# Optimization experiments

Measured on AMD Instinct MI355X. Metric: run time of the kernel, lower is better.

The kernel has to match this reference:

```python
import jax, jax.numpy as jnp
import numpy as np

DIM = 1024
N_HEADS = 16
HEAD_DIM = DIM // N_HEADS
B, N, M = 2, 2048, 2048


def setup_inputs() -> dict:
    key = jax.random.key(0)
    ks = jax.random.split(key, 10)
    s = 1.0 / np.sqrt(DIM)
    return {
        "x1": jax.random.normal(ks[0], (B, N, DIM), dtype=jnp.float32),
        "x2": jax.random.normal(ks[1], (B, M, DIM), dtype=jnp.float32),
        "Wq": jax.random.normal(ks[2], (DIM, DIM), dtype=jnp.float32) * s,
        "bq": jnp.zeros((DIM,), dtype=jnp.float32),
        "Wk": jax.random.normal(ks[3], (DIM, DIM), dtype=jnp.float32) * s,
        "bk": jnp.zeros((DIM,), dtype=jnp.float32),
        "Wv": jax.random.normal(ks[4], (DIM, DIM), dtype=jnp.float32) * s,
        "bv": jnp.zeros((DIM,), dtype=jnp.float32),
        "Wo": jax.random.normal(ks[5], (DIM, DIM), dtype=jnp.float32) * s,
        "bo": jnp.zeros((DIM,), dtype=jnp.float32),
    }


def reference(x1, x2, Wq, bq, Wk, bk, Wv, bv, Wo, bo):
    b, n, _ = x1.shape
    m = x2.shape[1]
    # projections (Linear: x @ W^T + b)
    q = x1 @ Wq.T + bq  # [b, n, dim]
    k = x2 @ Wk.T + bk  # [b, m, dim]
    v = x2 @ Wv.T + bv  # [b, m, dim]
    # split heads -> [b, h, seq, head_dim]
    q = q.reshape(b, n, N_HEADS, HEAD_DIM).transpose(0, 2, 1, 3)
    k = k.reshape(b, m, N_HEADS, HEAD_DIM).transpose(0, 2, 1, 3)
    v = v.reshape(b, m, N_HEADS, HEAD_DIM).transpose(0, 2, 1, 3)
    scale = 1.0 / jnp.sqrt(jnp.asarray(HEAD_DIM, dtype=q.dtype))
    scores = jnp.einsum('bhnd,bhmd->bhnm', q, k) * scale  # [b, h, n, m]
    attn = jax.nn.softmax(scores, axis=-1)
    o = jnp.einsum('bhnm,bhmd->bhnd', attn, v)  # [b, h, n, head_dim]
    o = o.transpose(0, 2, 1, 3).reshape(b, n, DIM)  # merge heads
    return o @ Wo.T + bo
```

## Files before the change

kernel.cpp:

```cpp
#include <hip/hip_runtime.h>
#include <stdint.h>

typedef unsigned short u16;
typedef __attribute__((ext_vector_type(4))) float f32x4;
typedef __attribute__((ext_vector_type(16))) float f32x16;
typedef __attribute__((ext_vector_type(8))) __bf16 bf16x8;
typedef __attribute__((ext_vector_type(8))) unsigned short u16x8;
typedef __attribute__((ext_vector_type(4))) unsigned short u16x4;

#define DIM_    1024
#define NHEADS_ 16
#define HD_     64
#define BB_     2
#define NN_     2048
#define MM_     2048

#define QSCALE 0.180336884f

__device__ inline u16 f32_to_bf16u(float f) {
  union { float f; uint32_t u; } x; x.f = f;
  uint32_t r = x.u + 0x7FFFu + ((x.u >> 16) & 1u);
  return (u16)(r >> 16);
}

__device__ inline void gload_lds16(const u16* g, u16* l) {
  u16* gnc = const_cast<u16*>(g);
  __builtin_amdgcn_global_load_lds(
      (__attribute__((address_space(1))) void*)gnc,
      (__attribute__((address_space(3))) void*)l, 16, 0, 0);
}

__device__ inline uint32_t cvt_pk_bf16(float lo, float hi) {
  uint32_t r;
  asm("v_cvt_pk_bf16_f32 %0, %1, %2" : "=v"(r) : "v"(lo), "v"(hi));
  return r;
}
__device__ inline void permlane32_swap(uint32_t& a, uint32_t& b) {
  asm("v_permlane32_swap_b32 %0, %1" : "+v"(a), "+v"(b));
}

__global__ void cast_all(const float* s0, u16* d0, const float* s1, u16* d1,
                         const float* s2, u16* d2, const float* s3, u16* d3,
                         const float* s4, u16* d4, const float* s5, u16* d5) {
  const float* s; u16* d; int n4;
  switch (blockIdx.y) {
    case 0: s = s0; d = d0; n4 = (BB_ * NN_ * DIM_) / 4; break;
    case 1: s = s1; d = d1; n4 = (BB_ * MM_ * DIM_) / 4; break;
    case 2: s = s2; d = d2; n4 = (DIM_ * DIM_) / 4; break;
    case 3: s = s3; d = d3; n4 = (DIM_ * DIM_) / 4; break;
    case 4: s = s4; d = d4; n4 = (DIM_ * DIM_) / 4; break;
    default: s = s5; d = d5; n4 = (DIM_ * DIM_) / 4; break;
  }
  int stride = gridDim.x * blockDim.x;
  for (int i = blockIdx.x * blockDim.x + threadIdx.x; i < n4; i += stride) {
    float4 f = reinterpret_cast<const float4*>(s)[i];
    u16x4 u;
    u.x = f32_to_bf16u(f.x);
    u.y = f32_to_bf16u(f.y);
    u.z = f32_to_bf16u(f.z);
    u.w = f32_to_bf16u(f.w);
    reinterpret_cast<u16x4*>(d)[i] = u;
  }
}

#define BM 128
#define BN 128
#define BK 64

template <bool BF16OUT>
__device__ __forceinline__
void gemm_body(const u16* __restrict__ A, const u16* __restrict__ Bm,
               const float* __restrict__ bias, void* __restrict__ Cout,
               int M, int N, int K, float scale,
               u16* As , u16* Bs ) {
  const int tid  = threadIdx.x;
  const int lane = tid & 63;
  const int wid  = tid >> 6;
  const int wr = wid >> 2, wc = wid & 3;
  const int fr = lane & 15, fq = lane >> 4;
  const int bm = blockIdx.x, bn = blockIdx.y;
  const int lrow = lane >> 3;
  const int scol = (((lane & 7) ^ lrow) * 8);

  f32x4 acc[4][2];
  #pragma unroll
  for (int m = 0; m < 4; ++m)
    #pragma unroll
    for (int n = 0; n < 2; ++n)
      acc[m][n] = f32x4{0.f, 0.f, 0.f, 0.f};

  const int NT = K / BK;

  auto stage = [&](int buf, int t) {
    int k0 = t * BK;
    #pragma unroll
    for (int c = 0; c < 2; ++c) {
      int ch  = wid * 2 + c;
      int row = ch * 8 + lrow;
      gload_lds16(A  + (size_t)(bm * BM + row) * K + k0 + scol, &As[buf * BM * BK + ch * 512]);
      gload_lds16(Bm + (size_t)(bn * BN + row) * K + k0 + scol, &Bs[buf * BN * BK + ch * 512]);
    }
  };

  stage(0, 0);
  __syncthreads();
  int cur = 0;
  for (int t = 0; t < NT; ++t) {
    if (t + 1 < NT) stage(cur ^ 1, t + 1);
    #pragma unroll
    for (int ks = 0; ks < 2; ++ks) {
      bf16x8 af[4], bfr[2];
      #pragma unroll
      for (int m = 0; m < 4; ++m)
        af[m] = *reinterpret_cast<const bf16x8*>(
            &As[cur * BM * BK + (wr * 64 + m * 16 + fr) * BK + (((ks * 4 + fq) ^ (fr & 7)) * 8)]);
      #pragma unroll
      for (int n = 0; n < 2; ++n)
        bfr[n] = *reinterpret_cast<const bf16x8*>(
            &Bs[cur * BN * BK + (wc * 32 + n * 16 + fr) * BK + (((ks * 4 + fq) ^ (fr & 7)) * 8)]);
      __builtin_amdgcn_s_setprio(1);
      #pragma unroll
      for (int m = 0; m < 4; ++m)
        #pragma unroll
        for (int n = 0; n < 2; ++n)
          acc[m][n] = __builtin_amdgcn_mfma_f32_16x16x32_bf16(af[m], bfr[n], acc[m][n], 0, 0, 0);
      __builtin_amdgcn_s_setprio(0);
    }
    __syncthreads();
    cur ^= 1;
  }

  #pragma unroll
  for (int n = 0; n < 2; ++n) {
    int col = bn * BN + wc * 32 + n * 16 + fr;
    float bv = bias[col];
    #pragma unroll
    for (int m = 0; m < 4; ++m) {
      #pragma unroll
      for (int i = 0; i < 4; ++i) {
        int row = bm * BM + wr * 64 + m * 16 + fq * 4 + i;
        float v = (acc[m][n][i] + bv) * scale;
        if (BF16OUT)
          ((u16*)Cout)[(size_t)row * N + col] = f32_to_bf16u(v);
        else
          ((float*)Cout)[(size_t)row * N + col] = v;
      }
    }
  }
}

__global__ __launch_bounds__(512)
void gemm_qkv(const u16* __restrict__ x1b, const u16* __restrict__ x2b,
              const u16* __restrict__ Wqb, const float* __restrict__ bq, u16* qb,
              const u16* __restrict__ Wkb, const float* __restrict__ bk, u16* kb,
              const u16* __restrict__ Wvb, const float* __restrict__ bv, u16* vb) {
  __shared__ __align__(16) u16 As[2 * BM * BK];
  __shared__ __align__(16) u16 Bs[2 * BN * BK];
  const u16* A; const u16* W; const float* bias; u16* C; float scale;
  switch (blockIdx.z) {
    case 0:  A = x1b; W = Wqb; bias = bq; C = qb; scale = QSCALE; break;
    case 1:  A = x2b; W = Wkb; bias = bk; C = kb; scale = 1.0f;   break;
    default: A = x2b; W = Wvb; bias = bv; C = vb; scale = 1.0f;   break;
  }
  gemm_body<true>(A, W, bias, C, BB_ * NN_, DIM_, DIM_, scale, As, Bs);
}

__global__ __launch_bounds__(512)
void gemm_o(const u16* __restrict__ A, const u16* __restrict__ W,
            const float* __restrict__ bias, float* __restrict__ C) {
  __shared__ __align__(16) u16 As[2 * BM * BK];
  __shared__ __align__(16) u16 Bs[2 * BN * BK];
  gemm_body<false>(A, W, bias, C, BB_ * NN_, DIM_, DIM_, 1.0f, As, Bs);
}

#define QB 128
#define KVB 64

__global__ __launch_bounds__(512)
void attn_fwd(const u16* __restrict__ qg, const u16* __restrict__ kg,
              const u16* __restrict__ vg, u16* __restrict__ og) {
  __shared__ __align__(16) u16 Ks[4][KVB * HD_];
  __shared__ __align__(16) u16 VTs[4][HD_ * KVB];
  const int tid = threadIdx.x, lane = tid & 63, wid = tid >> 6;
  const int hi = lane >> 5;
  const int l31 = lane & 31;
  const int wq = wid >> 1, wk = wid & 1;

  int lin = blockIdx.x + gridDim.x * (blockIdx.y + gridDim.y * blockIdx.z);
  int xcd = lin & 7, slot = lin >> 3;
  int r = slot & 15, gg2 = slot >> 4;
  int g = xcd + 8 * gg2;
  int h = g & 15, b = g >> 4;

  const size_t base_q  = (size_t)b * NN_ * DIM_ + (size_t)h * HD_;
  const size_t base_kv = (size_t)b * MM_ * DIM_ + (size_t)h * HD_;
  const int lrow = lane >> 3;
  const int scol = (((lane & 7) ^ lrow) * 8);

  bf16x8 qf[4];
  const int qrow = r * QB + wq * 32 + l31;
  #pragma unroll
  for (int step = 0; step < 4; ++step)
    qf[step] = *reinterpret_cast<const bf16x8*>(
        qg + base_q + (size_t)qrow * DIM_ + step * 16 + hi * 8);

  f32x16 oacc[2];
  #pragma unroll
  for (int dgrp = 0; dgrp < 2; ++dgrp)
    #pragma unroll
    for (int rg = 0; rg < 16; ++rg) oacc[dgrp][rg] = 0.f;
  float l_run = 0.f;

  const int NT = MM_ / KVB;

  auto stageK = [&](int buf, int t) {
    int kv0 = t * KVB;
    int row = wid * 8 + lrow;
    gload_lds16(kg + base_kv + (size_t)(kv0 + row) * DIM_ + scol, &Ks[buf][wid * 512]);
  };
  auto loadV = [&](int t, u16x8& vpre) {
    int kv0 = t * KVB;
    vpre = *reinterpret_cast<const u16x8*>(vg + base_kv + (size_t)(kv0 + lane) * DIM_ + wid * 8);
  };
  auto writeVT = [&](int buf, const u16x8& vpre) {
    #pragma unroll
    for (int j = 0; j < 8; ++j)
      VTs[buf][(wid * 8 + j) * KVB + (((lane >> 3) ^ j) * 8) + (lane & 7)] = vpre[j];
  };

  union PB { uint32_t w[4]; bf16x8 v; };

  auto compute = [&](int buf) {
    f32x16 s;
    #pragma unroll
    for (int rg = 0; rg < 16; ++rg) s[rg] = 0.f;
    __builtin_amdgcn_s_setprio(1);
    #pragma unroll
    for (int step = 0; step < 4; ++step) {
      bf16x8 kf = *reinterpret_cast<const bf16x8*>(
          (const char*)&Ks[buf][0] + (wk * 32 + l31) * 128 + (((step * 2 + hi) ^ (lane & 7)) * 16));
      s = __builtin_amdgcn_mfma_f32_32x32x16_bf16(kf, qf[step], s, 0, 0, 0);
    }
    __builtin_amdgcn_s_setprio(0);

    float p[16];
    #pragma unroll
    for (int rg = 0; rg < 16; ++rg) p[rg] = __builtin_amdgcn_exp2f(s[rg]);
    float lp = 0.f;
    #pragma unroll
    for (int rg = 0; rg < 16; ++rg) lp += p[rg];
    l_run += lp;

    PB pb[2];
    #pragma unroll
    for (int u = 0; u < 2; ++u) {
      uint32_t x0 = cvt_pk_bf16(p[u * 8 + 0], p[u * 8 + 1]);
      uint32_t y0 = cvt_pk_bf16(p[u * 8 + 4], p[u * 8 + 5]);
      permlane32_swap(x0, y0);
      uint32_t x1 = cvt_pk_bf16(p[u * 8 + 2], p[u * 8 + 3]);
      uint32_t y1 = cvt_pk_bf16(p[u * 8 + 6], p[u * 8 + 7]);
      permlane32_swap(x1, y1);
      pb[u].w[0] = x0; pb[u].w[1] = x1; pb[u].w[2] = y0; pb[u].w[3] = y1;
    }

    __builtin_amdgcn_s_setprio(1);
    #pragma unroll
    for (int dgrp = 0; dgrp < 2; ++dgrp)
      #pragma unroll
      for (int u = 0; u < 2; ++u) {
        bf16x8 vf = *reinterpret_cast<const bf16x8*>(
            (const char*)&VTs[buf][0] + (dgrp * 32 + l31) * 128 +
            (((wk * 4 + u * 2 + hi) ^ (lane & 7)) * 16));
        oacc[dgrp] = __builtin_amdgcn_mfma_f32_32x32x16_bf16(vf, pb[u].v, oacc[dgrp], 0, 0, 0);
      }
    __builtin_amdgcn_s_setprio(0);
  };

  {
    u16x8 v0, v1;
    loadV(0, v0);
    loadV(1, v1);
    stageK(0, 0);
    stageK(1, 1);
    writeVT(0, v0);
    writeVT(1, v1);
    __syncthreads();
  }

  for (int it = 0; it < NT / 2; ++it) {
    int t0 = 2 * it;
    u16x8 vpre0, vpre1;
    bool pre = (t0 + 2 < NT);
    if (pre) {
      loadV(t0 + 2, vpre0);
      loadV(t0 + 3, vpre1);
      stageK((t0 + 2) & 3, t0 + 2);
      stageK((t0 + 3) & 3, t0 + 3);
    }
    compute(t0 & 3);
    compute((t0 + 1) & 3);
    if (pre) {
      writeVT((t0 + 2) & 3, vpre0);
      writeVT((t0 + 3) & 3, vpre1);
    }
    __syncthreads();
  }

  float* Od = (float*)&Ks[0][0];
  float* Ls = (float*)&VTs[0][0];
  u16*  Of  = (u16*)((char*)&VTs[0][0] + 1024);

  if (wk == 1) {
    #pragma unroll
    for (int dgrp = 0; dgrp < 2; ++dgrp)
      #pragma unroll
      for (int rg = 0; rg < 16; ++rg) {
        int d = dgrp * 32 + (rg & 3) + 8 * (rg >> 2) + 4 * hi;
        Od[(wq * 32 + l31) * 64 + d] = oacc[dgrp][rg];
      }
    Ls[wq * 64 + hi * 32 + l31] = l_run;
  }
  __syncthreads();
  if (wk == 0) {
    #pragma unroll
    for (int dgrp = 0; dgrp < 2; ++dgrp)
      #pragma unroll
      for (int rg = 0; rg < 16; ++rg) {
        int d = dgrp * 32 + (rg & 3) + 8 * (rg >> 2) + 4 * hi;
        oacc[dgrp][rg] += Od[(wq * 32 + l31) * 64 + d];
      }
    float lown = l_run + __shfl_xor(l_run, 32, 64);
    float lfull = lown + Ls[wq * 64 + l31] + Ls[wq * 64 + 32 + l31];
    float inv = 1.f / lfull;
    #pragma unroll
    for (int dgrp = 0; dgrp < 2; ++dgrp)
      #pragma unroll
      for (int rg = 0; rg < 16; ++rg) {
        int d = dgrp * 32 + (rg & 3) + 8 * (rg >> 2) + 4 * hi;
        Of[(wq * 32 + l31) * 64 + d] = f32_to_bf16u(oacc[dgrp][rg] * inv);
      }
  }
  __syncthreads();
  #pragma unroll
  for (int itr = 0; itr < 2; ++itr) {
    int idx = itr * 512 + tid;
    int qq = idx >> 3;
    int ck = idx & 7;
    u16x8 v = *reinterpret_cast<const u16x8*>(&Of[qq * 64 + ck * 8]);
    *reinterpret_cast<u16x8*>(og + base_q + (size_t)(r * QB + qq) * DIM_ + ck * 8) = v;
  }
}

extern "C" void kernel_launch(void* const* d_in, const int* in_sizes, int n_in,
                              void* d_out, int out_size, void* d_ws, size_t ws_size,
                              hipStream_t stream) {
  (void)in_sizes; (void)n_in; (void)out_size; (void)ws_size;
  const float* x1 = (const float*)d_in[0];
  const float* x2 = (const float*)d_in[1];
  const float* Wq = (const float*)d_in[2];
  const float* bq = (const float*)d_in[3];
  const float* Wk = (const float*)d_in[4];
  const float* bk = (const float*)d_in[5];
  const float* Wv = (const float*)d_in[6];
  const float* bv = (const float*)d_in[7];
  const float* Wo = (const float*)d_in[8];
  const float* bo = (const float*)d_in[9];
  float* out = (float*)d_out;

  char* ws = (char*)d_ws;
  u16* x1b = (u16*)(ws);
  u16* x2b = (u16*)(ws + (8u  << 20));
  u16* Wqb = (u16*)(ws + (16u << 20));
  u16* Wkb = (u16*)(ws + (18u << 20));
  u16* Wvb = (u16*)(ws + (20u << 20));
  u16* Wob = (u16*)(ws + (22u << 20));
  u16* qb  = (u16*)(ws + (24u << 20));
  u16* kb  = (u16*)(ws + (32u << 20));
  u16* vb  = (u16*)(ws + (40u << 20));
  u16* ob  = (u16*)(ws + (48u << 20));

  cast_all<<<dim3(512, 6), 256, 0, stream>>>(x1, x1b, x2, x2b, Wq, Wqb,
                                             Wk, Wkb, Wv, Wvb, Wo, Wob);

  const int Mrows = BB_ * NN_;
  dim3 gqkv(Mrows / BM, DIM_ / BN, 3);
  gemm_qkv<<<gqkv, 512, 0, stream>>>(x1b, x2b, Wqb, bq, qb, Wkb, bk, kb, Wvb, bv, vb);

  dim3 ga(NN_ / QB, NHEADS_, BB_);
  attn_fwd<<<ga, 512, 0, stream>>>(qb, kb, vb, ob);

  dim3 gg(Mrows / BM, DIM_ / BN);
  gemm_o<<<gg, 512, 0, stream>>>(ob, Wob, bo, out);
}
```

Baseline: 125.3 us.

## Use triple-buffered KV pipeline and MFMA-based row sums in attention

The attention kernel moves from a 4-buffer, two-tiles-per-iteration loop to a 3-buffer ring that processes one KV tile per iteration. That cuts LDS footprint from 64KB to 48KB, which may allow more blocks per CU. The softmax row-sum is now computed with an extra MFMA against a ones vector instead of VALU adds, and the epilogue LDS layouts are padded to reduce bank conflicts. In exchange there are twice as many barriers and an extra MFMA per tile.

```diff
diff --git a/kernel.cpp b/kernel.cpp
--- a/kernel.cpp
+++ b/kernel.cpp
@@ -179,8 +179,7 @@
 __global__ __launch_bounds__(512)
 void attn_fwd(const u16* __restrict__ qg, const u16* __restrict__ kg,
               const u16* __restrict__ vg, u16* __restrict__ og) {
-  __shared__ __align__(16) u16 Ks[4][KVB * HD_];
-  __shared__ __align__(16) u16 VTs[4][HD_ * KVB];
+  __shared__ __align__(16) u16 KVs[6 * KVB * HD_];
   const int tid = threadIdx.x, lane = tid & 63, wid = tid >> 6;
   const int hi = lane >> 5;
   const int l31 = lane & 31;
@@ -204,19 +203,26 @@
     qf[step] = *reinterpret_cast<const bf16x8*>(
         qg + base_q + (size_t)qrow * DIM_ + step * 16 + hi * 8);
 
+  bf16x8 onesf;
+  #pragma unroll
+  for (int j = 0; j < 8; ++j) onesf[j] = (__bf16)1.0f;
+
   f32x16 oacc[2];
   #pragma unroll
   for (int dgrp = 0; dgrp < 2; ++dgrp)
     #pragma unroll
     for (int rg = 0; rg < 16; ++rg) oacc[dgrp][rg] = 0.f;
-  float l_run = 0.f;
+  f32x16 lacc;
+  #pragma unroll
+  for (int rg = 0; rg < 16; ++rg) lacc[rg] = 0.f;
 
   const int NT = MM_ / KVB;
 
   auto stageK = [&](int buf, int t) {
     int kv0 = t * KVB;
     int row = wid * 8 + lrow;
-    gload_lds16(kg + base_kv + (size_t)(kv0 + row) * DIM_ + scol, &Ks[buf][wid * 512]);
+    gload_lds16(kg + base_kv + (size_t)(kv0 + row) * DIM_ + scol,
+                &KVs[buf * 4096 + wid * 512]);
   };
   auto loadV = [&](int t, u16x8& vpre) {
     int kv0 = t * KVB;
@@ -225,12 +231,14 @@
   auto writeVT = [&](int buf, const u16x8& vpre) {
     #pragma unroll
     for (int j = 0; j < 8; ++j)
-      VTs[buf][(wid * 8 + j) * KVB + (((lane >> 3) ^ j) * 8) + (lane & 7)] = vpre[j];
+      KVs[(3 + buf) * 4096 + (wid * 8 + j) * KVB + (((lane >> 3) ^ j) * 8) + (lane & 7)] = vpre[j];
   };
 
   union PB { uint32_t w[4]; bf16x8 v; };
 
   auto compute = [&](int buf) {
+    const u16* Kb = &KVs[buf * 4096];
+    const u16* Vb = &KVs[(3 + buf) * 4096];
     f32x16 s;
     #pragma unroll
     for (int rg = 0; rg < 16; ++rg) s[rg] = 0.f;
@@ -238,7 +246,7 @@
     #pragma unroll
     for (int step = 0; step < 4; ++step) {
       bf16x8 kf = *reinterpret_cast<const bf16x8*>(
-          (const char*)&Ks[buf][0] + (wk * 32 + l31) * 128 + (((step * 2 + hi) ^ (lane & 7)) * 16));
+          (const char*)Kb + (wk * 32 + l31) * 128 + (((step * 2 + hi) ^ (lane & 7)) * 16));
       s = __builtin_amdgcn_mfma_f32_32x32x16_bf16(kf, qf[step], s, 0, 0, 0);
     }
     __builtin_amdgcn_s_setprio(0);
@@ -246,10 +254,6 @@
     float p[16];
     #pragma unroll
     for (int rg = 0; rg < 16; ++rg) p[rg] = __builtin_amdgcn_exp2f(s[rg]);
-    float lp = 0.f;
-    #pragma unroll
-    for (int rg = 0; rg < 16; ++rg) lp += p[rg];
-    l_run += lp;
 
     PB pb[2];
     #pragma unroll
@@ -265,11 +269,14 @@
 
     __builtin_amdgcn_s_setprio(1);
     #pragma unroll
+    for (int u = 0; u < 2; ++u)
+      lacc = __builtin_amdgcn_mfma_f32_32x32x16_bf16(onesf, pb[u].v, lacc, 0, 0, 0);
+    #pragma unroll
     for (int dgrp = 0; dgrp < 2; ++dgrp)
       #pragma unroll
       for (int u = 0; u < 2; ++u) {
         bf16x8 vf = *reinterpret_cast<const bf16x8*>(
-            (const char*)&VTs[buf][0] + (dgrp * 32 + l31) * 128 +
+            (const char*)Vb + (dgrp * 32 + l31) * 128 +
             (((wk * 4 + u * 2 + hi) ^ (lane & 7)) * 16));
         oacc[dgrp] = __builtin_amdgcn_mfma_f32_32x32x16_bf16(vf, pb[u].v, oacc[dgrp], 0, 0, 0);
       }
@@ -287,28 +294,24 @@
     __syncthreads();
   }
 
-  for (int it = 0; it < NT / 2; ++it) {
-    int t0 = 2 * it;
-    u16x8 vpre0, vpre1;
-    bool pre = (t0 + 2 < NT);
+  int cur = 0, stg = 2;
+  for (int t = 0; t < NT; ++t) {
+    u16x8 vpre;
+    bool pre = (t + 2 < NT);
     if (pre) {
-      loadV(t0 + 2, vpre0);
-      loadV(t0 + 3, vpre1);
-      stageK((t0 + 2) & 3, t0 + 2);
-      stageK((t0 + 3) & 3, t0 + 3);
-    }
-    compute(t0 & 3);
-    compute((t0 + 1) & 3);
-    if (pre) {
-      writeVT((t0 + 2) & 3, vpre0);
-      writeVT((t0 + 3) & 3, vpre1);
-    }
+      loadV(t + 2, vpre);
+      stageK(stg, t + 2);
+    }
+    compute(cur);
+    if (pre) writeVT(stg, vpre);
     __syncthreads();
-  }
-
-  float* Od = (float*)&Ks[0][0];
-  float* Ls = (float*)&VTs[0][0];
-  u16*  Of  = (u16*)((char*)&VTs[0][0] + 1024);
+    cur = (cur == 2) ? 0 : cur + 1;
+    stg = (stg == 2) ? 0 : stg + 1;
+  }
+
+  float* Od = (float*)&KVs[0];
+  float* Ls = (float*)&KVs[0] + 128 * 65;
+  u16*  Of  = (u16*)&KVs[0];
 
   if (wk == 1) {
     #pragma unroll
@@ -316,28 +319,29 @@
       #pragma unroll
       for (int rg = 0; rg < 16; ++rg) {
         int d = dgrp * 32 + (rg & 3) + 8 * (rg >> 2) + 4 * hi;
-        Od[(wq * 32 + l31) * 64 + d] = oacc[dgrp][rg];
-      }
-    Ls[wq * 64 + hi * 32 + l31] = l_run;
+        Od[(wq * 32 + l31) * 65 + d] = oacc[dgrp][rg];
+      }
+    if (hi == 0) Ls[wq * 32 + l31] = lacc[0];
   }
   __syncthreads();
   if (wk == 0) {
+    float inv = 1.f / (lacc[0] + Ls[wq * 32 + l31]);
     #pragma unroll
     for (int dgrp = 0; dgrp < 2; ++dgrp)
       #pragma unroll
       for (int rg = 0; rg < 16; ++rg) {
         int d = dgrp * 32 + (rg & 3) + 8 * (rg >> 2) + 4 * hi;
-        oacc[dgrp][rg] += Od[(wq * 32 + l31) * 64 + d];
-      }
-    float lown = l_run + __shfl_xor(l_run, 32, 64);
-    float lfull = lown + Ls[wq * 64 + l31] + Ls[wq * 64 + 32 + l31];
-    float inv = 1.f / lfull;
+        oacc[dgrp][rg] = (oacc[dgrp][rg] + Od[(wq * 32 + l31) * 65 + d]) * inv;
+      }
+  }
+  __syncthreads();
+  if (wk == 0) {
     #pragma unroll
     for (int dgrp = 0; dgrp < 2; ++dgrp)
       #pragma unroll
       for (int rg = 0; rg < 16; ++rg) {
         int d = dgrp * 32 + (rg & 3) + 8 * (rg >> 2) + 4 * hi;
-        Of[(wq * 32 + l31) * 64 + d] = f32_to_bf16u(oacc[dgrp][rg] * inv);
+        Of[(wq * 32 + l31) * 68 + d] = f32_to_bf16u(oacc[dgrp][rg]);
       }
   }
   __syncthreads();
@@ -346,7 +350,7 @@
     int idx = itr * 512 + tid;
     int qq = idx >> 3;
     int ck = idx & 7;
-    u16x8 v = *reinterpret_cast<const u16x8*>(&Of[qq * 64 + ck * 8]);
+    u16x8 v = *reinterpret_cast<const u16x8*>(&Of[qq * 68 + ck * 8]);
     *reinterpret_cast<u16x8*>(og + base_q + (size_t)(r * QB + qq) * DIM_ + ck * 8) = v;
   }
 }
```

Result: faster. 117.2 us (-6.5%).
